# Optimization experiments

Measured on AMD Instinct MI355X. Metric: run time of the kernel, lower is better.

The kernel has to match this reference:

```python
import jax, jax.numpy as jnp
import numpy as np
from jax import lax

CONF_BIT = 8        # mantissa bits for block-floating-point
CONF_GROUP_SIZE = 36  # elements sharing one exponent


def bfp_quantize(x, bits=CONF_BIT, group_size=CONF_GROUP_SIZE):
    """Group-wise block-floating-point quantization (make_groups_tensor).
    Consecutive groups of `group_size` elements of the flattened tensor share
    the exponent of the group's max magnitude; mantissas are rounded to `bits` bits."""
    shape = x.shape
    flat = x.reshape(-1)
    n = flat.shape[0]
    pad = (-n) % group_size
    flat = jnp.pad(flat, (0, pad))
    g = flat.reshape(-1, group_size)
    max_abs = jnp.max(jnp.abs(g), axis=1, keepdims=True)
    # shared exponent = floor(log2(max|x|)); guard zero groups
    exp = jnp.floor(jnp.log2(jnp.where(max_abs > 0, max_abs, 1.0)))
    step = jnp.exp2(exp - (bits - 1))  # quantization step per group
    qmax = 2 ** (bits - 1) - 1
    q = jnp.clip(jnp.round(g / step), -(qmax + 1), qmax) * step
    q = jnp.where(max_abs > 0, q, 0.0)
    return q.reshape(-1)[:n].reshape(shape)


def setup_inputs() -> dict:
    key = jax.random.key(0)
    k1, k2, k3 = jax.random.split(key, 3)
    B, Cin, Cout, H, W, K = 32, 128, 128, 112, 112, 3
    x = jax.random.normal(k1, (B, Cin, H, W), dtype=jnp.float32)
    fan_in = Cin * K * K
    weight = jax.random.normal(k2, (Cout, Cin, K, K), dtype=jnp.float32) / np.sqrt(fan_in)
    bound = 1.0 / np.sqrt(fan_in)
    bias = jax.random.uniform(k3, (Cout,), dtype=jnp.float32, minval=-bound, maxval=bound)
    return {"x": x, "weight": weight, "bias": bias}


def reference(x, weight, bias):
    # BFP-quantize input and weight, then plain conv2d (stride=1, padding=1)
    xq = bfp_quantize(x)
    wq = bfp_quantize(weight)
    out = lax.conv_general_dilated(
        xq, wq,
        window_strides=(1, 1),
        padding=((1, 1), (1, 1)),
        dimension_numbers=("NCHW", "OIHW", "NCHW"),
    )
    return out + bias[None, :, None, None]
```

## Files before the change

### kernel.cpp

```cpp
#include <hip/hip_runtime.h>

typedef __attribute__((ext_vector_type(8))) short short8;
typedef __attribute__((ext_vector_type(4))) float f32x4;

#define NB     32
#define NC     128
#define HW     112
#define PLANE  12544
#define XTOT   51380224
#define NGX    1427229
#define PADW   114
#define PADPLANE 12996
#define XPAD_BYTES 106463232ULL
#define WG_OFF     XPAD_BYTES
#define SE_OFF     (XPAD_BYTES + 294912ULL)

__device__ __forceinline__ void gld_lds16(const void* g, void* l) {
  __builtin_amdgcn_global_load_lds(
      (__attribute__((address_space(1))) unsigned int*)g,
      (__attribute__((address_space(3))) unsigned int*)l, 16, 0, 0);
}

__device__ __forceinline__ float qmax4(float4 v, float m) {
  m = fmaxf(m, fabsf(v.x)); m = fmaxf(m, fabsf(v.y));
  m = fmaxf(m, fabsf(v.z)); m = fmaxf(m, fabsf(v.w));
  return m;
}

__device__ __forceinline__ int bfp_exp(float m) {
  int e = 0;
  if (m > 0.f) {
    e = (int)((__float_as_uint(m) >> 23) & 255) - 127;
    if (e < -100) e = -100;
  }
  return e;
}

__device__ __forceinline__ unsigned short bfp_q(float v, float inv, float st) {
  float qq = fminf(fmaxf(rintf(v * inv), -128.f), 127.f) * st;
  return (unsigned short)(__float_as_uint(qq) >> 16);
}

__device__ __forceinline__ float mk_inv(int e) {
  return __uint_as_float((unsigned)(134 - e) << 23);
}
__device__ __forceinline__ float mk_st(int e) {
  return __uint_as_float((unsigned)(120 + e) << 23);
}

__global__ __launch_bounds__(256) void quant_step_x(const float* __restrict__ x,
                                                    signed char* __restrict__ se) {
  __shared__ float lds[9216];
  const int t = threadIdx.x;
  const int base = blockIdx.x * 9216;
  const float4* src = (const float4*)(x + base);
  const int rem4 = (XTOT - base) >> 2;
#pragma unroll
  for (int j = 0; j < 9; ++j) {
    int idx = j * 256 + t;
    float4 v = make_float4(0.f, 0.f, 0.f, 0.f);
    if (idx < rem4) v = src[idx];
    ((float4*)lds)[idx] = v;
  }
  __syncthreads();
  int g = blockIdx.x * 256 + t;
  if (g >= NGX) return;
  const float4* p4 = (const float4*)(lds + t * 36);
  float m = 0.f;
#pragma unroll
  for (int j = 0; j < 9; ++j) m = qmax4(p4[j], m);
  se[g] = (signed char)bfp_exp(m);
}

__global__ __launch_bounds__(256) void quant_w_kernel(const float* __restrict__ w,
                                                      unsigned short* __restrict__ wg) {
  __shared__ float wl[9216];
  __shared__ float wi[256], wsr[256];
  const int blk = blockIdx.x;
  const int t = threadIdx.x;
  const int base = blk * 9216;
  const float4* src = (const float4*)(w + base);
#pragma unroll
  for (int j = 0; j < 9; ++j) ((float4*)wl)[j * 256 + t] = src[j * 256 + t];
  __syncthreads();
  {
    const float4* p4 = (const float4*)(wl + t * 36);
    float m = 0.f;
#pragma unroll
    for (int j = 0; j < 9; ++j) m = qmax4(p4[j], m);
    int e = bfp_exp(m);
    wi[t] = mk_inv(e); wsr[t] = mk_st(e);
  }
  __syncthreads();
  const int cloc = t >> 5, cil = t & 31;
  const int co = blk * 8 + cloc;
#pragma unroll
  for (int stp = 0; stp < 36; ++stp) {
    int cib = stp & 3, rs = stp >> 2;
    int ci = cib * 32 + cil;
    int fl = cloc * 1152 + ci * 9 + rs;
    int g = fl / 36;
    wg[(stp * 128 + co) * 32 + cil] = bfp_q(wl[fl], wi[g], wsr[g]);
  }
}

#define TSTR 136
__global__ __launch_bounds__(256) void quant_pad_x(const float* __restrict__ x,
                                                   const signed char* __restrict__ se,
                                                   unsigned short* __restrict__ xpad) {
  __shared__ unsigned short tile[32 * TSTR];
  __shared__ float4 ist4[128];
  __shared__ unsigned char roll[128];
  int b = blockIdx.y;
  int p0 = blockIdx.x * 32;
  int t = threadIdx.x;

  int hid = (blockIdx.y * 392 + blockIdx.x) * 256 + t;
  if (hid < NB * 452 * 16) {
    int hb = hid / (452 * 16);
    int r = hid % (452 * 16);
    int pos = r >> 4, cc = r & 15;
    int hp, wp;
    if (pos < 114)      { hp = 0;             wp = pos; }
    else if (pos < 228) { hp = 113;           wp = pos - 114; }
    else if (pos < 340) { hp = pos - 228 + 1; wp = 0; }
    else                { hp = pos - 340 + 1; wp = 113; }
    float4 z = make_float4(0.f, 0.f, 0.f, 0.f);
    *(float4*)&xpad[((size_t)((hb * 114 + hp) * 114 + wp)) * 128 + cc * 8] = z;
  }

  if (t < 128) {
    int ci = t;
    int f0 = (b * 128 + ci) * PLANE + p0;
    int g = f0 / 36;
    int rem = f0 - g * 36;
    roll[ci] = (unsigned char)(36 - rem);
    int g1 = g + 1; if (g1 > NGX - 1) g1 = NGX - 1;
    int e0 = se[g], e1 = se[g1];
    ist4[ci] = make_float4(mk_inv(e0), mk_st(e0), mk_inv(e1), mk_st(e1));
  }
  __syncthreads();

  int pq  = (t & 7) * 4;
  int ci0 = (t >> 3) * 4;
  unsigned short q[4][4];
#pragma unroll
  for (int i = 0; i < 4; ++i) {
    int ci = ci0 + i;
    int f = (b * 128 + ci) * PLANE + p0 + pq;
    float4 v = *(const float4*)(x + f);
    float vv[4] = {v.x, v.y, v.z, v.w};
    float4 is_ = ist4[ci];
    int rl = roll[ci];
#pragma unroll
    for (int j = 0; j < 4; ++j) {
      bool sec = (pq + j) >= rl;
      float inv = sec ? is_.z : is_.x;
      float st  = sec ? is_.w : is_.y;
      q[i][j] = bfp_q(vv[j], inv, st);
    }
  }
#pragma unroll
  for (int j = 0; j < 4; ++j)
    *(ushort4*)&tile[(pq + j) * TSTR + ci0] = make_ushort4(q[0][j], q[1][j], q[2][j], q[3][j]);
  __syncthreads();
  int pl = t >> 3;
  int cc = t & 7;
  int p = p0 + pl;
  int h = p / 112, w = p % 112;
  float4 v0 = *(const float4*)&tile[pl * TSTR + cc * 16];
  float4 v1 = *(const float4*)&tile[pl * TSTR + cc * 16 + 8];
  size_t dst = ((size_t)((b * 114 + h + 1) * 114 + (w + 1))) * 128 + cc * 16;
  *(float4*)&xpad[dst]     = v0;
  *(float4*)&xpad[dst + 8] = v1;
}

__global__ __launch_bounds__(256) void conv_mfma(const unsigned short* __restrict__ xpad,
                                                 const unsigned short* __restrict__ wg,
                                                 const float* __restrict__ bias,
                                                 float* __restrict__ out) {
  __shared__ __align__(16) char smb[3 * 8192];
  const int t = threadIdx.x;
  const int lane = t & 63, wv = t >> 6;
  const int lane15 = lane & 15, quad = lane >> 4;
  const int wm = wv >> 1, wn = wv & 1;
  const int b = blockIdx.y;
  const int p0 = blockIdx.x * 128;

  int b_src[2];
#pragma unroll
  for (int i = 0; i < 2; ++i) {
    int idx = t + i * 256;
    int row = idx >> 2;
    int c = idx & 3;
    int sw = (row >> 1) & 3;
    int p = p0 + row;
    int h = p / 112, ww = p % 112;
    b_src[i] = ((b * 114 + h) * 114 + ww) * 128 + (c ^ sw) * 8;
  }

  int b_off[4];
#pragma unroll
  for (int f = 0; f < 4; ++f) {
    int prow = wn * 64 + f * 16 + lane15;
    b_off[f] = prow * 64 + ((quad ^ ((prow >> 1) & 3)) * 16);
  }

  int a_goff[4];
#pragma unroll
  for (int f = 0; f < 4; ++f)
    a_goff[f] = (wm * 64 + f * 16 + lane15) * 32 + quad * 8;

  f32x4 acc[4][4];
  f32x4 zero = {0.f, 0.f, 0.f, 0.f};
#pragma unroll
  for (int i = 0; i < 4; ++i)
#pragma unroll
    for (int j = 0; j < 4; ++j) acc[i][j] = zero;

  auto stage = [&](int step, char* dst) {
    int rs = step >> 2, cib = step & 3;
    int r = (rs * 11) >> 5;
    int s = rs - r * 3;
    int bofs = (r * 114 + s) * 128 + cib * 32;
#pragma unroll
    for (int i = 0; i < 2; ++i)
      gld_lds16(xpad + b_src[i] + bofs, dst + wv * 1024 + i * 4096);
  };

  auto loadA = [&](int step, short8* ar) {
    const unsigned short* wp_ = wg + step * 4096;
#pragma unroll
    for (int f = 0; f < 4; ++f) ar[f] = *(const short8*)(wp_ + a_goff[f]);
  };

  auto compute = [&](const char* sb, const short8* ar) {
    short8 bf[4];
#pragma unroll
    for (int f = 0; f < 4; ++f) bf[f] = *(const short8*)(sb + b_off[f]);
    __builtin_amdgcn_s_setprio(1);
#pragma unroll
    for (int i = 0; i < 4; ++i)
#pragma unroll
      for (int j = 0; j < 4; ++j)
        acc[i][j] = __builtin_amdgcn_mfma_f32_16x16x32_bf16(ar[i], bf[j], acc[i][j], 0, 0, 0);
    __builtin_amdgcn_s_setprio(0);
  };

  short8 areg[2][4];
  loadA(0, areg[0]);
  stage(0, smb);
  stage(1, smb + 8192);

#pragma unroll
  for (int T = 0; T < 36; ++T) {
    asm volatile("s_waitcnt vmcnt(2)\n\ts_barrier" ::: "memory");
    loadA(T + 1 < 36 ? T + 1 : 35, areg[(T + 1) & 1]);
    stage(T + 2 < 36 ? T + 2 : 35, smb + ((T + 2) % 3) * 8192);
    compute(smb + (T % 3) * 8192, areg[T & 1]);
  }

#pragma unroll
  for (int i = 0; i < 4; ++i)
#pragma unroll
    for (int j = 0; j < 4; ++j) {
      int p = p0 + wn * 64 + j * 16 + lane15;
#pragma unroll
      for (int rr = 0; rr < 4; ++rr) {
        int co = wm * 64 + i * 16 + quad * 4 + rr;
        out[(b * 128 + co) * PLANE + p] = acc[i][j][rr] + bias[co];
      }
    }
}

extern "C" void kernel_launch(void* const* d_in, const int* in_sizes, int n_in,
                              void* d_out, int out_size, void* d_ws, size_t ws_size,
                              hipStream_t stream) {
  const float* x    = (const float*)d_in[0];
  const float* w    = (const float*)d_in[1];
  const float* bias = (const float*)d_in[2];
  float* out = (float*)d_out;
  char* ws = (char*)d_ws;
  unsigned short* xpad = (unsigned short*)ws;
  unsigned short* wg   = (unsigned short*)(ws + WG_OFF);
  signed char*    se   = (signed char*)(ws + SE_OFF);

  quant_step_x<<<(NGX + 255) / 256, 256, 0, stream>>>(x, se);
  quant_w_kernel<<<16, 256, 0, stream>>>(w, wg);
  quant_pad_x<<<dim3(392, 32), 256, 0, stream>>>(x, se, xpad);
  conv_mfma<<<dim3(98, 32), 256, 0, stream>>>(xpad, wg, bias, out);
}
```

Baseline: 558.1 us.

## Deepen A-operand register prefetch to two steps and parallelize weight quantization

The conv main loop now keeps three A-fragment register buffers and prefetches weights two K-steps ahead, relaxing the wait count so global weight loads have more latency slack. The weight quantization kernel is restructured to one small block per output channel (128 blocks of 64 threads), replacing the division with a multiply-shift, so it spreads across more CUs. The extra register buffer raises VGPR pressure and could reduce occupancy in the MFMA kernel.

```diff
diff --git a/kernel.cpp b/kernel.cpp
--- a/kernel.cpp
+++ b/kernel.cpp
@@ -72,35 +72,38 @@
   se[g] = (signed char)bfp_exp(m);
 }
 
-__global__ __launch_bounds__(256) void quant_w_kernel(const float* __restrict__ w,
-                                                      unsigned short* __restrict__ wg) {
-  __shared__ float wl[9216];
-  __shared__ float wi[256], wsr[256];
-  const int blk = blockIdx.x;
+__global__ __launch_bounds__(64) void quant_w_kernel(const float* __restrict__ w,
+                                                     unsigned short* __restrict__ wg) {
+  __shared__ float4 wl4[288];
+  __shared__ float wi[32], wst[32];
+  const int co = blockIdx.x;
   const int t = threadIdx.x;
-  const int base = blk * 9216;
-  const float4* src = (const float4*)(w + base);
-#pragma unroll
-  for (int j = 0; j < 9; ++j) ((float4*)wl)[j * 256 + t] = src[j * 256 + t];
-  __syncthreads();
-  {
-    const float4* p4 = (const float4*)(wl + t * 36);
+  const float4* src = (const float4*)(w + co * 1152);
+  wl4[t]       = src[t];
+  wl4[t + 64]  = src[t + 64];
+  wl4[t + 128] = src[t + 128];
+  wl4[t + 192] = src[t + 192];
+  if (t < 32) wl4[t + 256] = src[t + 256];
+  __syncthreads();
+  if (t < 32) {
+    const float4* p4 = wl4 + t * 9;
     float m = 0.f;
 #pragma unroll
     for (int j = 0; j < 9; ++j) m = qmax4(p4[j], m);
     int e = bfp_exp(m);
-    wi[t] = mk_inv(e); wsr[t] = mk_st(e);
-  }
-  __syncthreads();
-  const int cloc = t >> 5, cil = t & 31;
-  const int co = blk * 8 + cloc;
-#pragma unroll
-  for (int stp = 0; stp < 36; ++stp) {
-    int cib = stp & 3, rs = stp >> 2;
-    int ci = cib * 32 + cil;
-    int fl = cloc * 1152 + ci * 9 + rs;
-    int g = fl / 36;
-    wg[(stp * 128 + co) * 32 + cil] = bfp_q(wl[fl], wi[g], wsr[g]);
+    wi[t] = mk_inv(e); wst[t] = mk_st(e);
+  }
+  __syncthreads();
+  const float* wl = (const float*)wl4;
+#pragma unroll
+  for (int k = 0; k < 18; ++k) {
+    int o = k * 64 + t;
+    int stp = o >> 5, cil = o & 31;
+    int ci = (stp & 3) * 32 + cil;
+    int rs = stp >> 2;
+    int fl = ci * 9 + rs;
+    int g = (fl * 1821) >> 16;
+    wg[stp * 4096 + co * 32 + cil] = bfp_q(wl[fl], wi[g], wst[g]);
   }
 }
 
@@ -247,17 +250,18 @@
     __builtin_amdgcn_s_setprio(0);
   };
 
-  short8 areg[2][4];
+  short8 areg[3][4];
   loadA(0, areg[0]);
   stage(0, smb);
+  loadA(1, areg[1]);
   stage(1, smb + 8192);
 
 #pragma unroll
   for (int T = 0; T < 36; ++T) {
-    asm volatile("s_waitcnt vmcnt(2)\n\ts_barrier" ::: "memory");
-    loadA(T + 1 < 36 ? T + 1 : 35, areg[(T + 1) & 1]);
+    asm volatile("s_waitcnt vmcnt(6)\n\ts_barrier" ::: "memory");
+    loadA(T + 2 < 36 ? T + 2 : 35, areg[(T + 2) % 3]);
     stage(T + 2 < 36 ? T + 2 : 35, smb + ((T + 2) % 3) * 8192);
-    compute(smb + (T % 3) * 8192, areg[T & 1]);
+    compute(smb + (T % 3) * 8192, areg[T % 3]);
   }
 
 #pragma unroll
@@ -286,7 +290,7 @@
   signed char*    se   = (signed char*)(ws + SE_OFF);
 
   quant_step_x<<<(NGX + 255) / 256, 256, 0, stream>>>(x, se);
-  quant_w_kernel<<<16, 256, 0, stream>>>(w, wg);
+  quant_w_kernel<<<128, 64, 0, stream>>>(w, wg);
   quant_pad_x<<<dim3(392, 32), 256, 0, stream>>>(x, se, xpad);
   conv_mfma<<<dim3(98, 32), 256, 0, stream>>>(xpad, wg, bias, out);
 }
```

New measurement: 557.5 us. No clear change (-0.1%).
